# Kernel tuning notes

Hardware: AMD Instinct MI355X
Metric: run time of the kernel (lower is better)

Reference implementation:

```python
import jax, jax.numpy as jnp
import numpy as np
import math

DIM = 1024
N_HEADS = 16
HEAD_DIM = DIM // N_HEADS
BS, SEQ, NNB = 8, 1024, 50
LN_EPS = 1e-12


def setup_inputs() -> dict:
    key = jax.random.key(0)
    ks = jax.random.split(key, 12)
    std = 0.02
    inp = {
        "x": jax.random.normal(ks[0], (BS, SEQ, DIM), jnp.float32),
        "x_neighbor": jax.random.normal(ks[1], (BS, NNB, DIM), jnp.float32),
        "mask": jnp.ones((BS, SEQ), jnp.int32),
        "neighbor_mask": jnp.ones((BS, NNB), jnp.float32),
        "qw": std * jax.random.normal(ks[2], (DIM, DIM), jnp.float32),
        "qb": jnp.zeros((DIM,), jnp.float32),
        "kw": std * jax.random.normal(ks[3], (DIM, DIM), jnp.float32),
        "kb": jnp.zeros((DIM,), jnp.float32),
        "vw": std * jax.random.normal(ks[4], (DIM, DIM), jnp.float32),
        "vb": jnp.zeros((DIM,), jnp.float32),
        "ow": std * jax.random.normal(ks[5], (DIM, DIM), jnp.float32),
        "ob": jnp.zeros((DIM,), jnp.float32),
        "ln_g": jnp.ones((DIM,), jnp.float32),
        "ln_b": jnp.zeros((DIM,), jnp.float32),
    }
    return inp


def _split_heads(t, bs):
    # [bs, s, dim] -> [bs, h, s, dh]
    return t.reshape(bs, -1, N_HEADS, HEAD_DIM).transpose(0, 2, 1, 3)


def reference(x, x_neighbor, mask, neighbor_mask, qw, qb, kw, kb, vw, vb, ow, ob, ln_g, ln_b):
    bs, seq, dim = x.shape
    # mean-pool neighbors with mask
    nm = neighbor_mask[..., None]                      # [bs, nnb, 1]
    xn = (x_neighbor * nm).sum(axis=1) / nm.sum(axis=1)  # [bs, dim]
    query = jnp.broadcast_to(xn[:, None, :], x.shape)    # [bs, seq, dim]

    q = _split_heads(query @ qw.T + qb, bs) / math.sqrt(HEAD_DIM)
    k = _split_heads(x @ kw.T + kb, bs)
    v = _split_heads(x @ vw.T + vb, bs)

    scores = jnp.einsum("bhqd,bhkd->bhqk", q, k)       # [bs, h, seq, seq]
    key_mask = (mask == 0)[:, None, None, :]            # [bs, 1, 1, seq]
    scores = jnp.where(key_mask, -jnp.inf, scores)
    weights = jax.nn.softmax(scores, axis=-1)           # dropout p=0.0 -> no-op
    context = jnp.einsum("bhqk,bhkd->bhqd", weights, v)
    context = context.transpose(0, 2, 1, 3).reshape(bs, seq, dim)
    out = context @ ow.T + ob

    h = out + x
    mu = h.mean(axis=-1, keepdims=True)
    var = ((h - mu) ** 2).mean(axis=-1, keepdims=True)
    return (h - mu) / jnp.sqrt(var + LN_EPS) * ln_g + ln_b
```

## Files before the change

### kernel.cpp

```cpp
#include <hip/hip_runtime.h>
#include <hip/hip_bf16.h>


#define DIM  1024
#define NH   16
#define HD   64
#define BS   8
#define SEQ  1024
#define NNB  50

#define OF_P     16
#define OF_NUMP  131088
#define OF_DENP  4325392
#define OF_XW    4329488
#define OF_CTX   4460560
#define OF_OUTR  4468752

__global__ void k_prep(const float* __restrict__ xnb, const float* __restrict__ nm,
                       const float* __restrict__ qw, const float* __restrict__ qb,
                       const float* __restrict__ kw, float* __restrict__ p){
  int h = blockIdx.x & 15, b = blockIdx.x >> 4;
  int tid = threadIdx.x, wv = tid >> 6, ln = tid & 63;
  __shared__ float xnl[1024];
  __shared__ float qp[256];
  __shared__ float ql[64];
  {
    int d = tid*4;
    float4 acc = {0,0,0,0}; float wsum = 0.f;
    #pragma unroll 10
    for (int n=0; n<NNB; n++){
      float w = nm[b*NNB + n];
      float4 v = *(const float4*)(xnb + (size_t)(b*NNB + n)*DIM + d);
      acc.x += w*v.x; acc.y += w*v.y; acc.z += w*v.z; acc.w += w*v.w;
      wsum += w;
    }
    float inv = 1.f/wsum;
    acc.x*=inv; acc.y*=inv; acc.z*=inv; acc.w*=inv;
    *(float4*)(xnl + d) = acc;
  }
  __syncthreads();
  {
    const float* qrow = qw + (size_t)(h*HD + ln)*DIM + wv*256;
    const float* xrow = xnl + wv*256;
    float part = 0.f;
    #pragma unroll 16
    for (int i=0; i<64; i++){
      float4 a = *(const float4*)(qrow + i*4);
      float4 c = *(const float4*)(xrow + i*4);
      part += a.x*c.x + a.y*c.y + a.z*c.z + a.w*c.w;
    }
    qp[wv*64 + ln] = part;
  }
  __syncthreads();
  if (wv == 0){
    float qv = qp[ln] + qp[64+ln] + qp[128+ln] + qp[192+ln];
    ql[ln] = (qv + qb[h*HD + ln]) * 0.125f;
  }
  __syncthreads();
  {
    int d = tid*4;
    float4 acc = {0,0,0,0};
    #pragma unroll 8
    for (int j=0; j<HD; j++){
      float qj = ql[j];
      float4 kv = *(const float4*)(kw + (size_t)(h*HD + j)*DIM + d);
      acc.x += qj*kv.x; acc.y += qj*kv.y; acc.z += qj*kv.z; acc.w += qj*kv.w;
    }
    *(float4*)(p + (size_t)(b*NH + h)*DIM + d) = acc;
  }
}

__global__ void k_swp(const float* __restrict__ x, const float* __restrict__ p,
                      const int* __restrict__ mask,
                      float* __restrict__ nump, float* __restrict__ denp){
  int b = blockIdx.x, sc = blockIdx.y;
  int s0 = sc * 32;
  int tid = threadIdx.x, wv = tid >> 6, ln = tid & 63;
  __shared__ float4 plds[256*5];
  __shared__ float  xlds[32*260];
  __shared__ float4 wlds[32*5];
  float* pf = (float*)plds;
  float* wf = (float*)wlds;

  int s = ln & 31, half = ln >> 5;
  float acc[4] = {0.f,0.f,0.f,0.f};
  for (int kc=0; kc<4; kc++){
    __syncthreads();
    #pragma unroll
    for (int it=0; it<16; it++){
      int idx = it*256 + tid;
      int d = idx & 255, h = idx >> 8;
      pf[d*20 + h] = p[(size_t)(b*NH + h)*DIM + kc*256 + d];
    }
    #pragma unroll
    for (int it=0; it<8; it++){
      int idx = it*256 + tid;
      int dd4 = idx & 63, ss = idx >> 6;
      float4 v = *(const float4*)(x + (size_t)(b*SEQ + s0 + ss)*DIM + kc*256 + dd4*4);
      *(float4*)(xlds + ss*260 + dd4*4) = v;
    }
    __syncthreads();
    #pragma unroll 8
    for (int dd4=0; dd4<32; dd4++){
      float4 xq = *(const float4*)(xlds + s*260 + half*128 + dd4*4);
      int dbase = (half*128 + dd4*4)*5 + wv;
      float4 p0 = plds[dbase], p1 = plds[dbase+5], p2 = plds[dbase+10], p3 = plds[dbase+15];
      acc[0] += xq.x*p0.x + xq.y*p1.x + xq.z*p2.x + xq.w*p3.x;
      acc[1] += xq.x*p0.y + xq.y*p1.y + xq.z*p2.y + xq.w*p3.y;
      acc[2] += xq.x*p0.z + xq.y*p1.z + xq.z*p2.z + xq.w*p3.z;
      acc[3] += xq.x*p0.w + xq.y*p1.w + xq.z*p2.w + xq.w*p3.w;
    }
  }
  #pragma unroll
  for (int u=0; u<4; u++) acc[u] += __shfl_xor(acc[u], 32, 64);
  if (ln < 32){
    float m = mask[b*SEQ + s0 + s] ? 1.f : 0.f;
    #pragma unroll
    for (int u=0; u<4; u++)
      wf[s*20 + wv*4 + u] = m * __expf(acc[u]);
  }
  __syncthreads();
  if (tid < 16){
    float dsum = 0.f;
    #pragma unroll
    for (int ss=0; ss<32; ss++) dsum += wf[ss*20 + tid];
    denp[(sc*BS + b)*NH + tid] = dsum;
  }
  int d = wv*256 + ln*4;
  const float* xbase = x + (size_t)(b*SEQ + s0)*DIM + d;
  float4 a[16];
  #pragma unroll
  for (int q=0; q<16; q++){ a[q].x=0.f; a[q].y=0.f; a[q].z=0.f; a[q].w=0.f; }
#define WACC(Q, WC) \
  a[Q].x += xq[u].x*(WC); a[Q].y += xq[u].y*(WC); a[Q].z += xq[u].z*(WC); a[Q].w += xq[u].w*(WC);
  for (int sb=0; sb<32; sb+=8){
    float4 xq[8];
    #pragma unroll
    for (int u=0; u<8; u++)
      xq[u] = *(const float4*)(xbase + (size_t)(sb+u)*DIM);
    #pragma unroll
    for (int u=0; u<8; u++){
      float4 w0 = wlds[(sb+u)*5 + 0];
      float4 w1 = wlds[(sb+u)*5 + 1];
      float4 w2 = wlds[(sb+u)*5 + 2];
      float4 w3 = wlds[(sb+u)*5 + 3];
      WACC(0,  w0.x) WACC(1,  w0.y) WACC(2,  w0.z) WACC(3,  w0.w)
      WACC(4,  w1.x) WACC(5,  w1.y) WACC(6,  w1.z) WACC(7,  w1.w)
      WACC(8,  w2.x) WACC(9,  w2.y) WACC(10, w2.z) WACC(11, w2.w)
      WACC(12, w3.x) WACC(13, w3.y) WACC(14, w3.z) WACC(15, w3.w)
    }
  }
#undef WACC
  float* dst = nump + (size_t)sc*(BS*NH*DIM) + (size_t)(b*NH)*DIM + d;
  #pragma unroll
  for (int q=0; q<16; q++)
    *(float4*)(dst + (size_t)q*DIM) = a[q];
}

__global__ void k_xwred(const float* __restrict__ nump, const float* __restrict__ denp,
                        float* __restrict__ xw){
  int id = blockIdx.x*256 + threadIdx.x;
  int bh = id >> 10;
  int b = bh >> 4, h = bh & 15;
  float den = 0.f;
  #pragma unroll
  for (int scn=0; scn<32; scn++) den += denp[(scn*BS + b)*NH + h];
  float num = 0.f;
  #pragma unroll
  for (int scn=0; scn<32; scn++) num += nump[(size_t)scn*(BS*NH*DIM) + id];
  xw[id] = num / den;
}

__global__ void k_ctx(const float* __restrict__ xw, const float* __restrict__ vw,
                      const float* __restrict__ vb, float* __restrict__ ctx){
  int wv = threadIdx.x >> 6, ln = threadIdx.x & 63;
  int jo = blockIdx.x*4 + wv;
  int h  = jo >> 6;
  float acc[BS] = {0,0,0,0,0,0,0,0};
  #pragma unroll
  for (int i=0; i<4; i++){
    int d = ln*4 + 256*i;
    float4 vv = *(const float4*)(vw + (size_t)jo*DIM + d);
    #pragma unroll
    for (int b=0; b<BS; b++){
      float4 xv = *(const float4*)(xw + (size_t)(b*NH + h)*DIM + d);
      acc[b] += vv.x*xv.x + vv.y*xv.y + vv.z*xv.z + vv.w*xv.w;
    }
  }
  #pragma unroll
  for (int off=32; off>=1; off>>=1){
    #pragma unroll
    for (int b=0; b<BS; b++) acc[b] += __shfl_down(acc[b], off, 64);
  }
  if (ln == 0){
    float bias = vb[jo];
    #pragma unroll
    for (int b=0; b<BS; b++) ctx[b*DIM + jo] = acc[b] + bias;
  }
}

__global__ void k_outrow(const float* __restrict__ ctx, const float* __restrict__ ow,
                         const float* __restrict__ ob, float* __restrict__ outr){
  int wv = threadIdx.x >> 6, ln = threadIdx.x & 63;
  int io = blockIdx.x*4 + wv;
  float acc[BS] = {0,0,0,0,0,0,0,0};
  #pragma unroll
  for (int i=0; i<4; i++){
    int d = ln*4 + 256*i;
    float4 wt = *(const float4*)(ow + (size_t)io*DIM + d);
    #pragma unroll
    for (int b=0; b<BS; b++){
      float4 cv = *(const float4*)(ctx + b*DIM + d);
      acc[b] += wt.x*cv.x + wt.y*cv.y + wt.z*cv.z + wt.w*cv.w;
    }
  }
  #pragma unroll
  for (int off=32; off>=1; off>>=1){
    #pragma unroll
    for (int b=0; b<BS; b++) acc[b] += __shfl_down(acc[b], off, 64);
  }
  if (ln == 0){
    float bias = ob[io];
    #pragma unroll
    for (int b=0; b<BS; b++) outr[b*DIM + io] = acc[b] + bias;
  }
}

__global__ void k_ln(const float* __restrict__ x, const float* __restrict__ outr,
                     const float* __restrict__ g, const float* __restrict__ bt,
                     float* __restrict__ out){
  int row = blockIdx.x;
  int b = row >> 10;
  size_t base = (size_t)row * DIM;
  int tid = threadIdx.x;
  float4 xv = ((const float4*)(x + base))[tid];
  float4 ov = ((const float4*)(outr + (size_t)b*DIM))[tid];
  float4 h;
  h.x = xv.x + ov.x; h.y = xv.y + ov.y; h.z = xv.z + ov.z; h.w = xv.w + ov.w;
  float s  = h.x + h.y + h.z + h.w;
  float s2 = h.x*h.x + h.y*h.y + h.z*h.z + h.w*h.w;
  #pragma unroll
  for (int off=32; off>=1; off>>=1){
    s  += __shfl_xor(s,  off, 64);
    s2 += __shfl_xor(s2, off, 64);
  }
  __shared__ float r1[4], r2[4];
  int wv = tid >> 6, ln = tid & 63;
  if (ln == 0){ r1[wv] = s; r2[wv] = s2; }
  __syncthreads();
  s  = r1[0] + r1[1] + r1[2] + r1[3];
  s2 = r2[0] + r2[1] + r2[2] + r2[3];
  float mu   = s  * (1.f/1024.f);
  float var  = s2 * (1.f/1024.f) - mu*mu;
  float rstd = rsqrtf(var + 1e-12f);
  float4 gv = ((const float4*)g)[tid];
  float4 bv = ((const float4*)bt)[tid];
  float4 y;
  y.x = (h.x - mu)*rstd*gv.x + bv.x;
  y.y = (h.y - mu)*rstd*gv.y + bv.y;
  y.z = (h.z - mu)*rstd*gv.z + bv.z;
  y.w = (h.w - mu)*rstd*gv.w + bv.w;
  ((float4*)(out + base))[tid] = y;
}

extern "C" void kernel_launch(void* const* d_in, const int* in_sizes, int n_in,
                              void* d_out, int out_size, void* d_ws, size_t ws_size,
                              hipStream_t stream) {
  const float* x    = (const float*)d_in[0];
  const float* xnb  = (const float*)d_in[1];
  const int*   mask = (const int*  )d_in[2];
  const float* nm   = (const float*)d_in[3];
  const float* qw   = (const float*)d_in[4];
  const float* qb   = (const float*)d_in[5];
  const float* kw   = (const float*)d_in[6];
  const float* vw   = (const float*)d_in[8];
  const float* vb   = (const float*)d_in[9];
  const float* ow   = (const float*)d_in[10];
  const float* ob   = (const float*)d_in[11];
  const float* lng  = (const float*)d_in[12];
  const float* lnb  = (const float*)d_in[13];
  float* out = (float*)d_out;

  float* ws   = (float*)d_ws;
  float* p    = ws + OF_P;
  float* nump = ws + OF_NUMP;
  float* denp = ws + OF_DENP;
  float* xw   = ws + OF_XW;
  float* ctx  = ws + OF_CTX;
  float* outr = ws + OF_OUTR;

  k_prep  <<<128,             256, 0, stream>>>(xnb, nm, qw, qb, kw, p);
  k_swp   <<<dim3(BS,32),     256, 0, stream>>>(x, p, mask, nump, denp);
  k_xwred <<<512,             256, 0, stream>>>(nump, denp, xw);
  k_ctx   <<<256,             256, 0, stream>>>(xw, vw, vb, ctx);
  k_outrow<<<256,             256, 0, stream>>>(ctx, ow, ob, outr);
  k_ln    <<<BS*SEQ,          256, 0, stream>>>(x, outr, lng, lnb, out);
}
```

Baseline: 182.0 us.

## Restructure k_swp to 1024-thread blocks reading x and p directly from global

The score/weighted-sum kernel now runs 1024 threads per block instead of 256. The score phase drops the LDS staging of p and x: each wave loads p rows and x rows straight from global into registers and reduces across lanes with shuffles. The weighted-sum phase splits heads across wave groups, so each thread keeps 4 accumulators instead of 16. This is meant to cut LDS traffic, syncs and register pressure and to raise parallelism. In exchange it adds a long shuffle-reduction chain and loads each x tile once per head group.

```diff
diff --git a/kernel.cpp b/kernel.cpp
--- a/kernel.cpp
+++ b/kernel.cpp
@@ -70,54 +70,66 @@
   }
 }
 
-__global__ void k_swp(const float* __restrict__ x, const float* __restrict__ p,
-                      const int* __restrict__ mask,
-                      float* __restrict__ nump, float* __restrict__ denp){
+__global__ __launch_bounds__(1024, 4)
+void k_swp(const float* __restrict__ x, const float* __restrict__ p,
+           const int* __restrict__ mask,
+           float* __restrict__ nump, float* __restrict__ denp){
   int b = blockIdx.x, sc = blockIdx.y;
   int s0 = sc * 32;
   int tid = threadIdx.x, wv = tid >> 6, ln = tid & 63;
-  __shared__ float4 plds[256*5];
-  __shared__ float  xlds[32*260];
-  __shared__ float4 wlds[32*5];
-  float* pf = (float*)plds;
-  float* wf = (float*)wlds;
-
-  int s = ln & 31, half = ln >> 5;
-  float acc[4] = {0.f,0.f,0.f,0.f};
+  __shared__ float wf[32*20];
+
+  int hg = wv & 3, sq = wv >> 2;
+  float acc[8][4];
+  #pragma unroll
+  for (int i=0; i<8; i++){ acc[i][0]=0.f; acc[i][1]=0.f; acc[i][2]=0.f; acc[i][3]=0.f; }
+
+  #pragma unroll 1
   for (int kc=0; kc<4; kc++){
-    __syncthreads();
-    #pragma unroll
-    for (int it=0; it<16; it++){
-      int idx = it*256 + tid;
-      int d = idx & 255, h = idx >> 8;
-      pf[d*20 + h] = p[(size_t)(b*NH + h)*DIM + kc*256 + d];
-    }
-    #pragma unroll
-    for (int it=0; it<8; it++){
-      int idx = it*256 + tid;
-      int dd4 = idx & 63, ss = idx >> 6;
-      float4 v = *(const float4*)(x + (size_t)(b*SEQ + s0 + ss)*DIM + kc*256 + dd4*4);
-      *(float4*)(xlds + ss*260 + dd4*4) = v;
-    }
-    __syncthreads();
-    #pragma unroll 8
-    for (int dd4=0; dd4<32; dd4++){
-      float4 xq = *(const float4*)(xlds + s*260 + half*128 + dd4*4);
-      int dbase = (half*128 + dd4*4)*5 + wv;
-      float4 p0 = plds[dbase], p1 = plds[dbase+5], p2 = plds[dbase+10], p3 = plds[dbase+15];
-      acc[0] += xq.x*p0.x + xq.y*p1.x + xq.z*p2.x + xq.w*p3.x;
-      acc[1] += xq.x*p0.y + xq.y*p1.y + xq.z*p2.y + xq.w*p3.y;
-      acc[2] += xq.x*p0.z + xq.y*p1.z + xq.z*p2.z + xq.w*p3.z;
-      acc[3] += xq.x*p0.w + xq.y*p1.w + xq.z*p2.w + xq.w*p3.w;
-    }
-  }
-  #pragma unroll
-  for (int u=0; u<4; u++) acc[u] += __shfl_xor(acc[u], 32, 64);
-  if (ln < 32){
-    float m = mask[b*SEQ + s0 + s] ? 1.f : 0.f;
-    #pragma unroll
-    for (int u=0; u<4; u++)
-      wf[s*20 + wv*4 + u] = m * __expf(acc[u]);
+    int d = kc*256 + ln*4;
+    const float* pb = p + (size_t)(b*NH + hg*4)*DIM + d;
+    float4 pr0 = *(const float4*)(pb);
+    float4 pr1 = *(const float4*)(pb +   (size_t)DIM);
+    float4 pr2 = *(const float4*)(pb + 2*(size_t)DIM);
+    float4 pr3 = *(const float4*)(pb + 3*(size_t)DIM);
+    const float* xb = x + (size_t)(b*SEQ + s0 + sq*8)*DIM + d;
+    #pragma unroll
+    for (int sb=0; sb<8; sb+=4){
+      float4 xr[4];
+      #pragma unroll
+      for (int u=0; u<4; u++)
+        xr[u] = *(const float4*)(xb + (size_t)(sb+u)*DIM);
+      #pragma unroll
+      for (int u=0; u<4; u++){
+        acc[sb+u][0] += xr[u].x*pr0.x + xr[u].y*pr0.y + xr[u].z*pr0.z + xr[u].w*pr0.w;
+        acc[sb+u][1] += xr[u].x*pr1.x + xr[u].y*pr1.y + xr[u].z*pr1.z + xr[u].w*pr1.w;
+        acc[sb+u][2] += xr[u].x*pr2.x + xr[u].y*pr2.y + xr[u].z*pr2.z + xr[u].w*pr2.w;
+        acc[sb+u][3] += xr[u].x*pr3.x + xr[u].y*pr3.y + xr[u].z*pr3.z + xr[u].w*pr3.w;
+      }
+    }
+  }
+  #pragma unroll
+  for (int off=1; off<64; off<<=1){
+    #pragma unroll
+    for (int si=0; si<8; si++){
+      acc[si][0] += __shfl_xor(acc[si][0], off, 64);
+      acc[si][1] += __shfl_xor(acc[si][1], off, 64);
+      acc[si][2] += __shfl_xor(acc[si][2], off, 64);
+      acc[si][3] += __shfl_xor(acc[si][3], off, 64);
+    }
+  }
+  if (ln == 0){
+    #pragma unroll
+    for (int si=0; si<8; si++){
+      float4 v; v.x = acc[si][0]; v.y = acc[si][1]; v.z = acc[si][2]; v.w = acc[si][3];
+      *(float4*)(wf + (sq*8 + si)*20 + hg*4) = v;
+    }
+  }
+  __syncthreads();
+  if (tid < 512){
+    int s = tid >> 4, h = tid & 15;
+    float sv = wf[s*20 + h];
+    wf[s*20 + h] = mask[b*SEQ + s0 + s] ? __expf(sv) : 0.f;
   }
   __syncthreads();
   if (tid < 16){
@@ -126,35 +138,30 @@
     for (int ss=0; ss<32; ss++) dsum += wf[ss*20 + tid];
     denp[(sc*BS + b)*NH + tid] = dsum;
   }
-  int d = wv*256 + ln*4;
+  int hg2 = wv >> 2, dc = wv & 3;
+  int d = dc*256 + ln*4;
   const float* xbase = x + (size_t)(b*SEQ + s0)*DIM + d;
-  float4 a[16];
-  #pragma unroll
-  for (int q=0; q<16; q++){ a[q].x=0.f; a[q].y=0.f; a[q].z=0.f; a[q].w=0.f; }
-#define WACC(Q, WC) \
-  a[Q].x += xq[u].x*(WC); a[Q].y += xq[u].y*(WC); a[Q].z += xq[u].z*(WC); a[Q].w += xq[u].w*(WC);
-  for (int sb=0; sb<32; sb+=8){
-    float4 xq[8];
-    #pragma unroll
-    for (int u=0; u<8; u++)
+  float4 a0={0,0,0,0}, a1={0,0,0,0}, a2={0,0,0,0}, a3={0,0,0,0};
+  #pragma unroll 2
+  for (int sb=0; sb<32; sb+=4){
+    float4 xq[4];
+    #pragma unroll
+    for (int u=0; u<4; u++)
       xq[u] = *(const float4*)(xbase + (size_t)(sb+u)*DIM);
     #pragma unroll
-    for (int u=0; u<8; u++){
-      float4 w0 = wlds[(sb+u)*5 + 0];
-      float4 w1 = wlds[(sb+u)*5 + 1];
-      float4 w2 = wlds[(sb+u)*5 + 2];
-      float4 w3 = wlds[(sb+u)*5 + 3];
-      WACC(0,  w0.x) WACC(1,  w0.y) WACC(2,  w0.z) WACC(3,  w0.w)
-      WACC(4,  w1.x) WACC(5,  w1.y) WACC(6,  w1.z) WACC(7,  w1.w)
-      WACC(8,  w2.x) WACC(9,  w2.y) WACC(10, w2.z) WACC(11, w2.w)
-      WACC(12, w3.x) WACC(13, w3.y) WACC(14, w3.z) WACC(15, w3.w)
-    }
-  }
-#undef WACC
-  float* dst = nump + (size_t)sc*(BS*NH*DIM) + (size_t)(b*NH)*DIM + d;
-  #pragma unroll
-  for (int q=0; q<16; q++)
-    *(float4*)(dst + (size_t)q*DIM) = a[q];
+    for (int u=0; u<4; u++){
+      float4 w = *(const float4*)(wf + (sb+u)*20 + hg2*4);
+      a0.x += xq[u].x*w.x; a0.y += xq[u].y*w.x; a0.z += xq[u].z*w.x; a0.w += xq[u].w*w.x;
+      a1.x += xq[u].x*w.y; a1.y += xq[u].y*w.y; a1.z += xq[u].z*w.y; a1.w += xq[u].w*w.y;
+      a2.x += xq[u].x*w.z; a2.y += xq[u].y*w.z; a2.z += xq[u].z*w.z; a2.w += xq[u].w*w.z;
+      a3.x += xq[u].x*w.w; a3.y += xq[u].y*w.w; a3.z += xq[u].z*w.w; a3.w += xq[u].w*w.w;
+    }
+  }
+  float* dst = nump + (size_t)sc*(BS*NH*DIM) + (size_t)(b*NH + hg2*4)*DIM + d;
+  *(float4*)(dst                 ) = a0;
+  *(float4*)(dst +   (size_t)DIM ) = a1;
+  *(float4*)(dst + 2*(size_t)DIM ) = a2;
+  *(float4*)(dst + 3*(size_t)DIM ) = a3;
 }
 
 __global__ void k_xwred(const float* __restrict__ nump, const float* __restrict__ denp,
@@ -289,10 +296,10 @@
   float* ctx  = ws + OF_CTX;
   float* outr = ws + OF_OUTR;
 
-  k_prep  <<<128,             256, 0, stream>>>(xnb, nm, qw, qb, kw, p);
-  k_swp   <<<dim3(BS,32),     256, 0, stream>>>(x, p, mask, nump, denp);
-  k_xwred <<<512,             256, 0, stream>>>(nump, denp, xw);
-  k_ctx   <<<256,             256, 0, stream>>>(xw, vw, vb, ctx);
-  k_outrow<<<256,             256, 0, stream>>>(ctx, ow, ob, outr);
-  k_ln    <<<BS*SEQ,          256, 0, stream>>>(x, outr, lng, lnb, out);
-}
+  k_prep  <<<128,             256,  0, stream>>>(xnb, nm, qw, qb, kw, p);
+  k_swp   <<<dim3(BS,32),     1024, 0, stream>>>(x, p, mask, nump, denp);
+  k_xwred <<<512,             256,  0, stream>>>(nump, denp, xw);
+  k_ctx   <<<256,             256,  0, stream>>>(xw, vw, vb, ctx);
+  k_outrow<<<256,             256,  0, stream>>>(ctx, ow, ob, outr);
+  k_ln    <<<BS*SEQ,          256,  0, stream>>>(x, outr, lng, lnb, out);
+}
```

Measured after the change: 173.4 us (median of 2 runs). 1.05x faster.
